# Performance work log

Hardware: AMD Instinct MI355X
Metric: run time of the kernel (lower is better)

Reference implementation:

```python
import jax, jax.numpy as jnp
import numpy as np

N = 50000
E = 800000
F = 128
H = 128
D = 3

def setup_inputs() -> dict:
    key = jax.random.key(0)
    ks = jax.random.split(key, 12)
    s = lambda fan_in: 1.0 / np.sqrt(fan_in)
    return {
        "node": jax.random.normal(ks[0], (N, F), jnp.float32),
        "coordinate": jax.random.normal(ks[1], (N, D), jnp.float32),
        "edge_index": jax.random.randint(ks[2], (2, E), 0, N, jnp.int32),
        "We1": jax.random.normal(ks[3], (2 * F + 1, H), jnp.float32) * s(2 * F + 1),
        "be1": jnp.zeros((H,), jnp.float32),
        "We2": jax.random.normal(ks[4], (H, H), jnp.float32) * s(H),
        "be2": jnp.zeros((H,), jnp.float32),
        "Wx": jax.random.normal(ks[5], (H, 1), jnp.float32) * s(H),
        "bx": jnp.zeros((1,), jnp.float32),
        "Wh1": jax.random.normal(ks[6], (F + H, H), jnp.float32) * s(F + H),
        "bh1": jnp.zeros((H,), jnp.float32),
        "Wh2": jax.random.normal(ks[7], (H, F), jnp.float32) * s(H),
        "bh2": jnp.zeros((F,), jnp.float32),
    }

def reference(node, coordinate, edge_index, We1, be1, We2, be2, Wx, bx, Wh1, bh1, Wh2, bh2):
    src = edge_index[0]
    dst = edge_index[1]
    n = node.shape[0]
    # gather endpoint features / coords
    h_j = node[src]            # [E, F]
    h_i = node[dst]            # [E, F]
    dist = coordinate[dst] - coordinate[src]          # [E, D] = x_i - x_j
    sqdist = jnp.sum(dist * dist, axis=1, keepdims=True)  # [E, 1]
    # phi_e: Linear -> ReLU -> Linear
    e_in = jnp.concatenate([h_i, h_j, sqdist], axis=-1)    # [E, 2F+1]
    m_ij = jax.nn.relu(e_in @ We1 + be1) @ We2 + be2       # [E, H]
    # phi_x: Linear to scalar edge weight
    w_ij = m_ij @ Wx + bx                                  # [E, 1]
    vec = dist * w_ij                                      # [E, D]
    C = 1.0 / (n - 1)
    delta_x = jax.ops.segment_sum(vec, dst, num_segments=n) * C
    x_new = coordinate + delta_x
    # aggregate messages per target node (sum)
    m_i = jax.ops.segment_sum(m_ij, dst, num_segments=n)   # [N, H]
    # phi_h: Linear -> ReLU -> Linear
    h_in = jnp.concatenate([node, m_i], axis=1)            # [N, F+H]
    h_new = jax.nn.relu(h_in @ Wh1 + bh1) @ Wh2 + bh2      # [N, F]
    return (h_new, x_new)
```

## Files before the change

kernel.cpp:

```cpp
#include <hip/hip_runtime.h>
#include <stdint.h>

#define NN 50000
#define NE 800000
#define NBINS 50001
#define H_OUT_OFF 6400000

typedef float  f32x4  __attribute__((ext_vector_type(4)));
typedef short  bf16x8 __attribute__((ext_vector_type(8)));

static __device__ __forceinline__ unsigned short f2b(float f) {
  unsigned u = __float_as_uint(f);
  return (unsigned short)((u + 0x7fffu + ((u >> 16) & 1u)) >> 16);
}
static __device__ __forceinline__ float b2f(unsigned short h) {
  return __uint_as_float(((unsigned)h) << 16);
}

__global__ void k1_kernel(const int* __restrict__ ei,
                          int* __restrict__ cnt,
                          unsigned short* __restrict__ rank,
                          const float* __restrict__ We1,
                          const float* __restrict__ We2,
                          const float* __restrict__ Wh1,
                          const float* __restrict__ Wh2,
                          const float* __restrict__ be2,
                          const float* __restrict__ Wx,
                          const float* __restrict__ bx,
                          unsigned short* __restrict__ We1Ttop,
                          unsigned short* __restrict__ We1Tbot,
                          unsigned short* __restrict__ We2T,
                          unsigned short* __restrict__ Wh1T,
                          unsigned short* __restrict__ Wh2T,
                          float* __restrict__ uvec) {
  int b = blockIdx.x, tid = threadIdx.x;
  if (b < 3125) {
    int i = b * 256 + tid;
    if (i < NE) rank[i] = (unsigned short)atomicAdd(&cnt[ei[NE + i]], 1);
    return;
  }
  b -= 3125;
  if (b < 384) {
    int i = b * 256 + tid;
    if (i < 16384) {
      int n = i >> 7, k = i & 127;
      We1Ttop[i] = f2b(We1[k * 128 + n]);
    } else if (i < 32768) {
      int j = i - 16384; int n = j >> 7, k = j & 127;
      We1Tbot[j] = f2b(We1[(128 + k) * 128 + n]);
    } else if (i < 49152) {
      int j = i - 32768; int n = j >> 7, k = j & 127;
      We2T[j] = f2b(We2[k * 128 + n]);
    } else if (i < 81920) {
      int j = i - 49152; int n = j >> 8, k = j & 255;
      Wh1T[j] = f2b(Wh1[k * 128 + n]);
    } else if (i < 98304) {
      int j = i - 81920; int n = j >> 7, k = j & 127;
      Wh2T[j] = f2b(Wh2[k * 128 + n]);
    }
    return;
  }
  int k = tid;
  if (k < 128) {
    float s = 0.f;
    for (int n = 0; n < 128; n++) s += We2[k * 128 + n] * Wx[n];
    uvec[k] = s;
  } else if (k == 128) {
    float s = 0.f;
    for (int n = 0; n < 128; n++) s += be2[n] * Wx[n];
    uvec[128] = s + bx[0];
  }
}

__global__ void scanA_kernel(const int* __restrict__ cnt, int* __restrict__ bsum) {
  __shared__ int sd[256];
  int b = blockIdx.x, t = threadIdx.x, i = b * 256 + t;
  sd[t] = (i < NBINS) ? cnt[i] : 0;
  __syncthreads();
  for (int s = 128; s; s >>= 1) {
    if (t < s) sd[t] += sd[t + s];
    __syncthreads();
  }
  if (t == 0) bsum[b] = sd[0];
}

__global__ void scanC_kernel(const int* __restrict__ cnt, const int* __restrict__ bsum,
                             int* __restrict__ starts) {
  __shared__ int sd[256];
  int b = blockIdx.x, t = threadIdx.x, i = b * 256 + t;
  int bv = (t < 196) ? bsum[t] : 0;
  sd[t] = bv;
  __syncthreads();
  for (int off = 1; off < 256; off <<= 1) {
    int x = (t >= off) ? sd[t - off] : 0;
    __syncthreads();
    sd[t] += x;
    __syncthreads();
  }
  int boff = (b > 0) ? sd[b - 1] : 0;
  __syncthreads();
  int v = (i < NBINS) ? cnt[i] : 0;
  sd[t] = v;
  __syncthreads();
  for (int off = 1; off < 256; off <<= 1) {
    int x = (t >= off) ? sd[t - off] : 0;
    __syncthreads();
    sd[t] += x;
    __syncthreads();
  }
  if (i < NBINS) starts[i] = sd[t] - v + boff;
}

__global__ __launch_bounds__(256, 4)
void k3_kernel(const int* __restrict__ ei,
               const unsigned short* __restrict__ rank,
               const int* __restrict__ starts,
               unsigned short* __restrict__ srcs,
               const float* __restrict__ node,
               const unsigned short* __restrict__ We1Ttop,
               const unsigned short* __restrict__ We1Tbot,
               const float* __restrict__ be1,
               unsigned short* __restrict__ Yb,
               unsigned short* __restrict__ Zb) {
  __shared__ __align__(16) unsigned short sA[64][136];
  const int tid = threadIdx.x;
  int b = blockIdx.x;

  if (b < 3125) {
    int i = b * 256 + tid;
    if (i < NE) {
      srcs[starts[ei[NE + i]] + (int)rank[i]] = (unsigned short)ei[i];
    }
    return;
  }
  b -= 3125;
  const int n0 = b * 64;

  for (int c = tid; c < 64 * 16; c += 256) {
    int e = c >> 4, s = c & 15;
    int n = n0 + e;
    if (n < NN) {
      const float* p = node + (size_t)n * 128 + s * 8;
      float4 v0 = *(const float4*)p;
      float4 v1 = *(const float4*)(p + 4);
      *(ushort4*)&sA[e][s * 8]     = make_ushort4(f2b(v0.x), f2b(v0.y), f2b(v0.z), f2b(v0.w));
      *(ushort4*)&sA[e][s * 8 + 4] = make_ushort4(f2b(v1.x), f2b(v1.y), f2b(v1.z), f2b(v1.w));
    } else {
      *(uint4*)&sA[e][s * 8] = make_uint4(0, 0, 0, 0);
    }
  }
  __syncthreads();

  const int wave = tid >> 6, lane = tid & 63;
  const int quad = lane >> 4, l16 = lane & 15;
  const int col0 = wave * 32 + l16, col1 = wave * 32 + 16 + l16;

  const f32x4 zero = {0.f, 0.f, 0.f, 0.f};
  f32x4 accY[4][2], accZ[4][2];
#pragma unroll
  for (int mt = 0; mt < 4; mt++) {
    accY[mt][0] = zero; accY[mt][1] = zero;
    accZ[mt][0] = zero; accZ[mt][1] = zero;
  }

#pragma unroll
  for (int kt = 0; kt < 4; kt++) {
    int kb = kt * 32 + quad * 8;
    bf16x8 by0 = *(const bf16x8*)(We1Ttop + (col0 << 7) + kb);
    bf16x8 by1 = *(const bf16x8*)(We1Ttop + (col1 << 7) + kb);
    bf16x8 bz0 = *(const bf16x8*)(We1Tbot + (col0 << 7) + kb);
    bf16x8 bz1 = *(const bf16x8*)(We1Tbot + (col1 << 7) + kb);
#pragma unroll
    for (int mt = 0; mt < 4; mt++) {
      bf16x8 a = *(const bf16x8*)&sA[mt * 16 + l16][kb];
      accY[mt][0] = __builtin_amdgcn_mfma_f32_16x16x32_bf16(a, by0, accY[mt][0], 0, 0, 0);
      accY[mt][1] = __builtin_amdgcn_mfma_f32_16x16x32_bf16(a, by1, accY[mt][1], 0, 0, 0);
      accZ[mt][0] = __builtin_amdgcn_mfma_f32_16x16x32_bf16(a, bz0, accZ[mt][0], 0, 0, 0);
      accZ[mt][1] = __builtin_amdgcn_mfma_f32_16x16x32_bf16(a, bz1, accZ[mt][1], 0, 0, 0);
    }
  }

  float sb0 = be1[col0], sb1 = be1[col1];
#pragma unroll
  for (int mt = 0; mt < 4; mt++) {
#pragma unroll
    for (int r = 0; r < 4; r++) {
      int row = mt * 16 + quad * 4 + r;
      int n = n0 + row;
      if (n < NN) {
        Yb[(size_t)n * 128 + col0] = f2b(accY[mt][0][r] + sb0);
        Yb[(size_t)n * 128 + col1] = f2b(accY[mt][1][r] + sb1);
        Zb[(size_t)n * 128 + col0] = f2b(accZ[mt][0][r]);
        Zb[(size_t)n * 128 + col1] = f2b(accZ[mt][1][r]);
      }
    }
  }
}

__global__ __launch_bounds__(256, 8)
void edge_kernel(const unsigned short* __restrict__ Zb,
                 const unsigned short* __restrict__ Yb,
                 const unsigned short* __restrict__ srcs,
                 const int* __restrict__ starts,
                 const float* __restrict__ coord,
                 const float* __restrict__ We1,
                 const float* __restrict__ uvec,
                 float* __restrict__ T,
                 float* __restrict__ out) {
  __shared__ int    sSrc[4][64];
  __shared__ float4 sQ[4][64];

  const int tid = threadIdx.x, wave = tid >> 6, lane = tid & 63;
  const int n = blockIdx.x * 4 + wave;
  const int half = lane >> 5, l32 = lane & 31;
  const int col = l32 * 4;

  const int start = starts[n], end = starts[n + 1];

  const float4 wsq = *(const float4*)(We1 + 256 * 128 + col);
  const float4 u   = *(const float4*)(uvec + col);
  const float  c   = uvec[128];
  ushort4 yv = *(const ushort4*)(Yb + (size_t)n * 128 + col);
  const float y0 = b2f(yv.x), y1 = b2f(yv.y), y2 = b2f(yv.z), y3 = b2f(yv.w);
  const float cdx = coord[n * 3 + 0], cdy = coord[n * 3 + 1], cdz = coord[n * 3 + 2];

  float aT0 = 0.f, aT1 = 0.f, aT2 = 0.f, aT3 = 0.f;
  float sx = 0.f, sy = 0.f, sz = 0.f;
  float dsx = 0.f, dsy = 0.f, dsz = 0.f;

  for (int cb = start; cb < end; cb += 64) {
    int m = end - cb; if (m > 64) m = 64;
    int s = 0; float dx = 0.f, dy = 0.f, dz = 0.f;
    if (lane < m) {
      s = (int)srcs[cb + lane];
      dx = cdx - coord[s * 3 + 0];
      dy = cdy - coord[s * 3 + 1];
      dz = cdz - coord[s * 3 + 2];
      dsx += dx; dsy += dy; dsz += dz;
    }
    sSrc[wave][lane] = s;
    sQ[wave][lane] = make_float4(dx, dy, dz, dx * dx + dy * dy + dz * dz);
    __builtin_amdgcn_wave_barrier();
    int pairs = (m + 1) >> 1;
    for (int p = 0; p < pairs; p++) {
      int idx = 2 * p + half;
      int ss = sSrc[wave][idx];
      float4 q = sQ[wave][idx];
      float valid = (idx < m) ? 1.f : 0.f;
      ushort4 zv = *(const ushort4*)(Zb + (size_t)ss * 128 + col);
      float t0 = fmaxf(b2f(zv.x) + y0 + q.w * wsq.x, 0.f) * valid;
      float t1 = fmaxf(b2f(zv.y) + y1 + q.w * wsq.y, 0.f) * valid;
      float t2 = fmaxf(b2f(zv.z) + y2 + q.w * wsq.z, 0.f) * valid;
      float t3 = fmaxf(b2f(zv.w) + y3 + q.w * wsq.w, 0.f) * valid;
      aT0 += t0; aT1 += t1; aT2 += t2; aT3 += t3;
      float tu = t0 * u.x + t1 * u.y + t2 * u.z + t3 * u.w;
      sx += tu * q.x; sy += tu * q.y; sz += tu * q.z;
    }
    __builtin_amdgcn_wave_barrier();
  }

  aT0 += __shfl_xor(aT0, 32); aT1 += __shfl_xor(aT1, 32);
  aT2 += __shfl_xor(aT2, 32); aT3 += __shfl_xor(aT3, 32);
  if (half == 0) {
    *(float4*)&T[(size_t)n * 128 + col] = make_float4(aT0, aT1, aT2, aT3);
  }

  float px = sx + c * dsx, py = sy + c * dsy, pz = sz + c * dsz;
#pragma unroll
  for (int o = 1; o < 64; o <<= 1) {
    px += __shfl_xor(px, o); py += __shfl_xor(py, o); pz += __shfl_xor(pz, o);
  }
  if (lane == 0) {
    const float C = 1.0f / 49999.0f;
    out[H_OUT_OFF + n * 3 + 0] = cdx + C * px;
    out[H_OUT_OFF + n * 3 + 1] = cdy + C * py;
    out[H_OUT_OFF + n * 3 + 2] = cdz + C * pz;
  }
}

__global__ __launch_bounds__(256, 3)
void node_kernel(const float* __restrict__ node,
                 const float* __restrict__ T,
                 const int* __restrict__ starts,
                 const unsigned short* __restrict__ We2T,
                 const float* __restrict__ be2,
                 const unsigned short* __restrict__ Wh1T,
                 const float* __restrict__ bh1,
                 const unsigned short* __restrict__ Wh2T,
                 const float* __restrict__ bh2,
                 float* __restrict__ out) {
  __shared__ __align__(16) unsigned short sA[64][264];
  __shared__ __align__(16) unsigned short sT[64][136];
  __shared__ float sDeg[64];

  const int tid = threadIdx.x;
  const int n0 = blockIdx.x * 64;

  if (tid < 64) {
    int n = n0 + tid;
    sDeg[tid] = (n < NN) ? (float)(starts[n + 1] - starts[n]) : 0.f;
  }

  for (int c = tid; c < 64 * 16; c += 256) {
    int e = c >> 4, s = c & 15;
    int n = n0 + e;
    if (n < NN) {
      const float* pn = node + (size_t)n * 128 + s * 8;
      float4 a0 = *(const float4*)pn;
      float4 a1 = *(const float4*)(pn + 4);
      *(ushort4*)&sA[e][s * 8]     = make_ushort4(f2b(a0.x), f2b(a0.y), f2b(a0.z), f2b(a0.w));
      *(ushort4*)&sA[e][s * 8 + 4] = make_ushort4(f2b(a1.x), f2b(a1.y), f2b(a1.z), f2b(a1.w));
      const float* p = T + (size_t)n * 128 + s * 8;
      float4 v0 = *(const float4*)p;
      float4 v1 = *(const float4*)(p + 4);
      *(ushort4*)&sT[e][s * 8]     = make_ushort4(f2b(v0.x), f2b(v0.y), f2b(v0.z), f2b(v0.w));
      *(ushort4*)&sT[e][s * 8 + 4] = make_ushort4(f2b(v1.x), f2b(v1.y), f2b(v1.z), f2b(v1.w));
    } else {
      *(uint4*)&sA[e][s * 8] = make_uint4(0, 0, 0, 0);
      *(uint4*)&sT[e][s * 8] = make_uint4(0, 0, 0, 0);
    }
  }
  __syncthreads();

  const int wave = tid >> 6, lane = tid & 63;
  const int quad = lane >> 4, l16 = lane & 15;
  const int col0 = wave * 32 + l16, col1 = wave * 32 + 16 + l16;

  const f32x4 zero = {0.f, 0.f, 0.f, 0.f};

  f32x4 accM[4][2];
#pragma unroll
  for (int mt = 0; mt < 4; mt++) { accM[mt][0] = zero; accM[mt][1] = zero; }
#pragma unroll
  for (int kt = 0; kt < 4; kt++) {
    int kb = kt * 32 + quad * 8;
    bf16x8 b0 = *(const bf16x8*)(We2T + (col0 << 7) + kb);
    bf16x8 b1 = *(const bf16x8*)(We2T + (col1 << 7) + kb);
#pragma unroll
    for (int mt = 0; mt < 4; mt++) {
      bf16x8 a = *(const bf16x8*)&sT[mt * 16 + l16][kb];
      accM[mt][0] = __builtin_amdgcn_mfma_f32_16x16x32_bf16(a, b0, accM[mt][0], 0, 0, 0);
      accM[mt][1] = __builtin_amdgcn_mfma_f32_16x16x32_bf16(a, b1, accM[mt][1], 0, 0, 0);
    }
  }
  {
    float eb0 = be2[col0], eb1 = be2[col1];
#pragma unroll
    for (int mt = 0; mt < 4; mt++) {
#pragma unroll
      for (int r = 0; r < 4; r++) {
        int row = mt * 16 + quad * 4 + r;
        float dg = sDeg[row];
        sA[row][128 + col0] = f2b(accM[mt][0][r] + dg * eb0);
        sA[row][128 + col1] = f2b(accM[mt][1][r] + dg * eb1);
      }
    }
  }
  __syncthreads();

  f32x4 acc[4][2];
#pragma unroll
  for (int mt = 0; mt < 4; mt++) { acc[mt][0] = zero; acc[mt][1] = zero; }
#pragma unroll
  for (int kt = 0; kt < 8; kt++) {
    int kb = kt * 32 + quad * 8;
    bf16x8 b0 = *(const bf16x8*)(Wh1T + (col0 << 8) + kb);
    bf16x8 b1 = *(const bf16x8*)(Wh1T + (col1 << 8) + kb);
#pragma unroll
    for (int mt = 0; mt < 4; mt++) {
      bf16x8 a = *(const bf16x8*)&sA[mt * 16 + l16][kb];
      acc[mt][0] = __builtin_amdgcn_mfma_f32_16x16x32_bf16(a, b0, acc[mt][0], 0, 0, 0);
      acc[mt][1] = __builtin_amdgcn_mfma_f32_16x16x32_bf16(a, b1, acc[mt][1], 0, 0, 0);
    }
  }
  {
    float sb0 = bh1[col0], sb1 = bh1[col1];
#pragma unroll
    for (int mt = 0; mt < 4; mt++) {
#pragma unroll
      for (int r = 0; r < 4; r++) {
        int row = mt * 16 + quad * 4 + r;
        sT[row][col0] = f2b(fmaxf(acc[mt][0][r] + sb0, 0.f));
        sT[row][col1] = f2b(fmaxf(acc[mt][1][r] + sb1, 0.f));
      }
    }
  }
  __syncthreads();

  f32x4 acc2[4][2];
#pragma unroll
  for (int mt = 0; mt < 4; mt++) { acc2[mt][0] = zero; acc2[mt][1] = zero; }
#pragma unroll
  for (int kt = 0; kt < 4; kt++) {
    int kb = kt * 32 + quad * 8;
    bf16x8 b0 = *(const bf16x8*)(Wh2T + (col0 << 7) + kb);
    bf16x8 b1 = *(const bf16x8*)(Wh2T + (col1 << 7) + kb);
#pragma unroll
    for (int mt = 0; mt < 4; mt++) {
      bf16x8 a = *(const bf16x8*)&sT[mt * 16 + l16][kb];
      acc2[mt][0] = __builtin_amdgcn_mfma_f32_16x16x32_bf16(a, b0, acc2[mt][0], 0, 0, 0);
      acc2[mt][1] = __builtin_amdgcn_mfma_f32_16x16x32_bf16(a, b1, acc2[mt][1], 0, 0, 0);
    }
  }
  {
    float eb0 = bh2[col0], eb1 = bh2[col1];
#pragma unroll
    for (int mt = 0; mt < 4; mt++) {
#pragma unroll
      for (int r = 0; r < 4; r++) {
        int row = mt * 16 + quad * 4 + r;
        int n = n0 + row;
        if (n < NN) {
          out[(size_t)n * 128 + col0] = acc2[mt][0][r] + eb0;
          out[(size_t)n * 128 + col1] = acc2[mt][1][r] + eb1;
        }
      }
    }
  }
}

extern "C" void kernel_launch(void* const* d_in, const int* in_sizes, int n_in,
                              void* d_out, int out_size, void* d_ws, size_t ws_size,
                              hipStream_t stream) {
  const float* node  = (const float*)d_in[0];
  const float* coord = (const float*)d_in[1];
  const int*   ei    = (const int*)d_in[2];
  const float* We1   = (const float*)d_in[3];
  const float* be1   = (const float*)d_in[4];
  const float* We2   = (const float*)d_in[5];
  const float* be2   = (const float*)d_in[6];
  const float* Wx    = (const float*)d_in[7];
  const float* bx    = (const float*)d_in[8];
  const float* Wh1   = (const float*)d_in[9];
  const float* bh1   = (const float*)d_in[10];
  const float* Wh2   = (const float*)d_in[11];
  const float* bh2   = (const float*)d_in[12];
  float* out = (float*)d_out;

  char* ws = (char*)d_ws;
  float*          T      = (float*)(ws);
  int*            cnt    = (int*)  (ws + 25600000);
  int*            starts = (int*)  (ws + 25800704);
  int*            bsum   = (int*)  (ws + 26001408);
  unsigned short* rank   = (unsigned short*)(ws + 26002432);
  unsigned short* srcs   = (unsigned short*)(ws + 27602432);
  unsigned short* Yb     = (unsigned short*)(ws + 29202432);
  unsigned short* Zb     = (unsigned short*)(ws + 42002432);
  unsigned short* We1Ttop= (unsigned short*)(ws + 54802432);
  unsigned short* We1Tbot= (unsigned short*)(ws + 54835200);
  unsigned short* We2T   = (unsigned short*)(ws + 54867968);
  unsigned short* Wh1T   = (unsigned short*)(ws + 54900736);
  unsigned short* Wh2T   = (unsigned short*)(ws + 54966272);
  float*          uvec   = (float*)(ws + 54999040);

  hipMemsetAsync(cnt, 0, 200704, stream);

  k1_kernel<<<3510, 256, 0, stream>>>(ei, cnt, rank, We1, We2, Wh1, Wh2,
                                      be2, Wx, bx,
                                      We1Ttop, We1Tbot, We2T, Wh1T, Wh2T, uvec);
  scanA_kernel<<<196, 256, 0, stream>>>(cnt, bsum);
  scanC_kernel<<<196, 256, 0, stream>>>(cnt, bsum, starts);
  k3_kernel<<<3907, 256, 0, stream>>>(ei, rank, starts, srcs,
                                      node, We1Ttop, We1Tbot, be1, Yb, Zb);
  edge_kernel<<<NN / 4, 256, 0, stream>>>(Zb, Yb, srcs, starts, coord, We1, uvec,
                                          T, out);
  node_kernel<<<782, 256, 0, stream>>>(node, T, starts, We2T, be2,
                                       Wh1T, bh1, Wh2T, bh2, out);
}
```

Baseline: 242.0 us.

## Fuse edge aggregation into node MLP kernel, keeping aggregates in shared memory

Merges the per-node edge aggregation kernel with the node MLP kernel. Each block first gathers and sums messages for its 64 nodes (one wave per 16 nodes sequentially), writing the aggregated bf16 features into shared memory alongside the node features. It then runs the MLP chain, which removes the fp32 T round-trip through global memory and one launch. The trade is far fewer waves working on the latency-bound gather, plus extra barriers from reusing the shared buffer.

```diff
diff --git a/kernel.cpp b/kernel.cpp
--- a/kernel.cpp
+++ b/kernel.cpp
@@ -17,15 +17,11 @@
   return __uint_as_float(((unsigned)h) << 16);
 }
 
-__global__ void k1_kernel(const int* __restrict__ ei,
-                          int* __restrict__ cnt,
+__global__ void k1_kernel(const int* __restrict__ ei, int* __restrict__ cnt,
                           unsigned short* __restrict__ rank,
-                          const float* __restrict__ We1,
-                          const float* __restrict__ We2,
-                          const float* __restrict__ Wh1,
-                          const float* __restrict__ Wh2,
-                          const float* __restrict__ be2,
-                          const float* __restrict__ Wx,
+                          const float* __restrict__ We1, const float* __restrict__ We2,
+                          const float* __restrict__ Wh1, const float* __restrict__ Wh2,
+                          const float* __restrict__ be2, const float* __restrict__ Wx,
                           const float* __restrict__ bx,
                           unsigned short* __restrict__ We1Ttop,
                           unsigned short* __restrict__ We1Tbot,
@@ -112,30 +108,23 @@
 }
 
 __global__ __launch_bounds__(256, 4)
-void k3_kernel(const int* __restrict__ ei,
-               const unsigned short* __restrict__ rank,
-               const int* __restrict__ starts,
-               unsigned short* __restrict__ srcs,
+void k3_kernel(const int* __restrict__ ei, const unsigned short* __restrict__ rank,
+               const int* __restrict__ starts, unsigned short* __restrict__ srcs,
                const float* __restrict__ node,
                const unsigned short* __restrict__ We1Ttop,
                const unsigned short* __restrict__ We1Tbot,
                const float* __restrict__ be1,
-               unsigned short* __restrict__ Yb,
-               unsigned short* __restrict__ Zb) {
+               unsigned short* __restrict__ Yb, unsigned short* __restrict__ Zb) {
   __shared__ __align__(16) unsigned short sA[64][136];
   const int tid = threadIdx.x;
   int b = blockIdx.x;
-
   if (b < 3125) {
     int i = b * 256 + tid;
-    if (i < NE) {
-      srcs[starts[ei[NE + i]] + (int)rank[i]] = (unsigned short)ei[i];
-    }
+    if (i < NE) srcs[starts[ei[NE + i]] + (int)rank[i]] = (unsigned short)ei[i];
     return;
   }
   b -= 3125;
   const int n0 = b * 64;
-
   for (int c = tid; c < 64 * 16; c += 256) {
     int e = c >> 4, s = c & 15;
     int n = n0 + e;
@@ -150,11 +139,9 @@
     }
   }
   __syncthreads();
-
   const int wave = tid >> 6, lane = tid & 63;
   const int quad = lane >> 4, l16 = lane & 15;
   const int col0 = wave * 32 + l16, col1 = wave * 32 + 16 + l16;
-
   const f32x4 zero = {0.f, 0.f, 0.f, 0.f};
   f32x4 accY[4][2], accZ[4][2];
 #pragma unroll
@@ -162,7 +149,6 @@
     accY[mt][0] = zero; accY[mt][1] = zero;
     accZ[mt][0] = zero; accZ[mt][1] = zero;
   }
-
 #pragma unroll
   for (int kt = 0; kt < 4; kt++) {
     int kb = kt * 32 + quad * 8;
@@ -179,7 +165,6 @@
       accZ[mt][1] = __builtin_amdgcn_mfma_f32_16x16x32_bf16(a, bz1, accZ[mt][1], 0, 0, 0);
     }
   }
-
   float sb0 = be1[col0], sb1 = be1[col1];
 #pragma unroll
   for (int mt = 0; mt < 4; mt++) {
@@ -197,109 +182,29 @@
   }
 }
 
-__global__ __launch_bounds__(256, 8)
-void edge_kernel(const unsigned short* __restrict__ Zb,
-                 const unsigned short* __restrict__ Yb,
-                 const unsigned short* __restrict__ srcs,
-                 const int* __restrict__ starts,
-                 const float* __restrict__ coord,
-                 const float* __restrict__ We1,
-                 const float* __restrict__ uvec,
-                 float* __restrict__ T,
-                 float* __restrict__ out) {
+__global__ __launch_bounds__(256, 4)
+void en_kernel(const unsigned short* __restrict__ Zb,
+               const unsigned short* __restrict__ Yb,
+               const unsigned short* __restrict__ srcs,
+               const int* __restrict__ starts,
+               const float* __restrict__ coord,
+               const float* __restrict__ We1,
+               const float* __restrict__ uvec,
+               const float* __restrict__ node,
+               const unsigned short* __restrict__ We2T,
+               const float* __restrict__ be2,
+               const unsigned short* __restrict__ Wh1T,
+               const float* __restrict__ bh1,
+               const unsigned short* __restrict__ Wh2T,
+               const float* __restrict__ bh2,
+               float* __restrict__ out) {
+  __shared__ __align__(16) unsigned short sA[64][264];
+  __shared__ float  sDeg[64];
   __shared__ int    sSrc[4][64];
   __shared__ float4 sQ[4][64];
 
   const int tid = threadIdx.x, wave = tid >> 6, lane = tid & 63;
-  const int n = blockIdx.x * 4 + wave;
-  const int half = lane >> 5, l32 = lane & 31;
-  const int col = l32 * 4;
-
-  const int start = starts[n], end = starts[n + 1];
-
-  const float4 wsq = *(const float4*)(We1 + 256 * 128 + col);
-  const float4 u   = *(const float4*)(uvec + col);
-  const float  c   = uvec[128];
-  ushort4 yv = *(const ushort4*)(Yb + (size_t)n * 128 + col);
-  const float y0 = b2f(yv.x), y1 = b2f(yv.y), y2 = b2f(yv.z), y3 = b2f(yv.w);
-  const float cdx = coord[n * 3 + 0], cdy = coord[n * 3 + 1], cdz = coord[n * 3 + 2];
-
-  float aT0 = 0.f, aT1 = 0.f, aT2 = 0.f, aT3 = 0.f;
-  float sx = 0.f, sy = 0.f, sz = 0.f;
-  float dsx = 0.f, dsy = 0.f, dsz = 0.f;
-
-  for (int cb = start; cb < end; cb += 64) {
-    int m = end - cb; if (m > 64) m = 64;
-    int s = 0; float dx = 0.f, dy = 0.f, dz = 0.f;
-    if (lane < m) {
-      s = (int)srcs[cb + lane];
-      dx = cdx - coord[s * 3 + 0];
-      dy = cdy - coord[s * 3 + 1];
-      dz = cdz - coord[s * 3 + 2];
-      dsx += dx; dsy += dy; dsz += dz;
-    }
-    sSrc[wave][lane] = s;
-    sQ[wave][lane] = make_float4(dx, dy, dz, dx * dx + dy * dy + dz * dz);
-    __builtin_amdgcn_wave_barrier();
-    int pairs = (m + 1) >> 1;
-    for (int p = 0; p < pairs; p++) {
-      int idx = 2 * p + half;
-      int ss = sSrc[wave][idx];
-      float4 q = sQ[wave][idx];
-      float valid = (idx < m) ? 1.f : 0.f;
-      ushort4 zv = *(const ushort4*)(Zb + (size_t)ss * 128 + col);
-      float t0 = fmaxf(b2f(zv.x) + y0 + q.w * wsq.x, 0.f) * valid;
-      float t1 = fmaxf(b2f(zv.y) + y1 + q.w * wsq.y, 0.f) * valid;
-      float t2 = fmaxf(b2f(zv.z) + y2 + q.w * wsq.z, 0.f) * valid;
-      float t3 = fmaxf(b2f(zv.w) + y3 + q.w * wsq.w, 0.f) * valid;
-      aT0 += t0; aT1 += t1; aT2 += t2; aT3 += t3;
-      float tu = t0 * u.x + t1 * u.y + t2 * u.z + t3 * u.w;
-      sx += tu * q.x; sy += tu * q.y; sz += tu * q.z;
-    }
-    __builtin_amdgcn_wave_barrier();
-  }
-
-  aT0 += __shfl_xor(aT0, 32); aT1 += __shfl_xor(aT1, 32);
-  aT2 += __shfl_xor(aT2, 32); aT3 += __shfl_xor(aT3, 32);
-  if (half == 0) {
-    *(float4*)&T[(size_t)n * 128 + col] = make_float4(aT0, aT1, aT2, aT3);
-  }
-
-  float px = sx + c * dsx, py = sy + c * dsy, pz = sz + c * dsz;
-#pragma unroll
-  for (int o = 1; o < 64; o <<= 1) {
-    px += __shfl_xor(px, o); py += __shfl_xor(py, o); pz += __shfl_xor(pz, o);
-  }
-  if (lane == 0) {
-    const float C = 1.0f / 49999.0f;
-    out[H_OUT_OFF + n * 3 + 0] = cdx + C * px;
-    out[H_OUT_OFF + n * 3 + 1] = cdy + C * py;
-    out[H_OUT_OFF + n * 3 + 2] = cdz + C * pz;
-  }
-}
-
-__global__ __launch_bounds__(256, 3)
-void node_kernel(const float* __restrict__ node,
-                 const float* __restrict__ T,
-                 const int* __restrict__ starts,
-                 const unsigned short* __restrict__ We2T,
-                 const float* __restrict__ be2,
-                 const unsigned short* __restrict__ Wh1T,
-                 const float* __restrict__ bh1,
-                 const unsigned short* __restrict__ Wh2T,
-                 const float* __restrict__ bh2,
-                 float* __restrict__ out) {
-  __shared__ __align__(16) unsigned short sA[64][264];
-  __shared__ __align__(16) unsigned short sT[64][136];
-  __shared__ float sDeg[64];
-
-  const int tid = threadIdx.x;
   const int n0 = blockIdx.x * 64;
-
-  if (tid < 64) {
-    int n = n0 + tid;
-    sDeg[tid] = (n < NN) ? (float)(starts[n + 1] - starts[n]) : 0.f;
-  }
 
   for (int c = tid; c < 64 * 16; c += 256) {
     int e = c >> 4, s = c & 15;
@@ -310,22 +215,93 @@
       float4 a1 = *(const float4*)(pn + 4);
       *(ushort4*)&sA[e][s * 8]     = make_ushort4(f2b(a0.x), f2b(a0.y), f2b(a0.z), f2b(a0.w));
       *(ushort4*)&sA[e][s * 8 + 4] = make_ushort4(f2b(a1.x), f2b(a1.y), f2b(a1.z), f2b(a1.w));
-      const float* p = T + (size_t)n * 128 + s * 8;
-      float4 v0 = *(const float4*)p;
-      float4 v1 = *(const float4*)(p + 4);
-      *(ushort4*)&sT[e][s * 8]     = make_ushort4(f2b(v0.x), f2b(v0.y), f2b(v0.z), f2b(v0.w));
-      *(ushort4*)&sT[e][s * 8 + 4] = make_ushort4(f2b(v1.x), f2b(v1.y), f2b(v1.z), f2b(v1.w));
     } else {
       *(uint4*)&sA[e][s * 8] = make_uint4(0, 0, 0, 0);
-      *(uint4*)&sT[e][s * 8] = make_uint4(0, 0, 0, 0);
-    }
-  }
-  __syncthreads();
-
-  const int wave = tid >> 6, lane = tid & 63;
+    }
+  }
+
+  {
+    const int half = lane >> 5, l32 = lane & 31;
+    const int col = l32 * 4;
+    const float4 wsq = *(const float4*)(We1 + 256 * 128 + col);
+    const float4 u   = *(const float4*)(uvec + col);
+    const float  cc  = uvec[128];
+
+    for (int r16 = 0; r16 < 16; r16++) {
+      const int row = (wave << 4) + r16;
+      const int n = n0 + row;
+      if (n < NN) {
+        const int start = starts[n], end = starts[n + 1];
+        ushort4 yv = *(const ushort4*)(Yb + (size_t)n * 128 + col);
+        const float y0 = b2f(yv.x), y1 = b2f(yv.y), y2 = b2f(yv.z), y3 = b2f(yv.w);
+        const float cdx = coord[n * 3 + 0], cdy = coord[n * 3 + 1], cdz = coord[n * 3 + 2];
+
+        float aT0 = 0.f, aT1 = 0.f, aT2 = 0.f, aT3 = 0.f;
+        float sx = 0.f, sy = 0.f, sz = 0.f;
+        float dsx = 0.f, dsy = 0.f, dsz = 0.f;
+
+        for (int cb = start; cb < end; cb += 64) {
+          int m = end - cb; if (m > 64) m = 64;
+          int s = 0; float dx = 0.f, dy = 0.f, dz = 0.f;
+          if (lane < m) {
+            s = (int)srcs[cb + lane];
+            dx = cdx - coord[s * 3 + 0];
+            dy = cdy - coord[s * 3 + 1];
+            dz = cdz - coord[s * 3 + 2];
+            dsx += dx; dsy += dy; dsz += dz;
+          }
+          sSrc[wave][lane] = s;
+          sQ[wave][lane] = make_float4(dx, dy, dz, dx * dx + dy * dy + dz * dz);
+          __builtin_amdgcn_wave_barrier();
+          int pairs = (m + 1) >> 1;
+          for (int p = 0; p < pairs; p++) {
+            int idx = 2 * p + half;
+            int ss = sSrc[wave][idx];
+            float4 q = sQ[wave][idx];
+            float valid = (idx < m) ? 1.f : 0.f;
+            ushort4 zv = *(const ushort4*)(Zb + (size_t)ss * 128 + col);
+            float t0 = fmaxf(b2f(zv.x) + y0 + q.w * wsq.x, 0.f) * valid;
+            float t1 = fmaxf(b2f(zv.y) + y1 + q.w * wsq.y, 0.f) * valid;
+            float t2 = fmaxf(b2f(zv.z) + y2 + q.w * wsq.z, 0.f) * valid;
+            float t3 = fmaxf(b2f(zv.w) + y3 + q.w * wsq.w, 0.f) * valid;
+            aT0 += t0; aT1 += t1; aT2 += t2; aT3 += t3;
+            float tu = t0 * u.x + t1 * u.y + t2 * u.z + t3 * u.w;
+            sx += tu * q.x; sy += tu * q.y; sz += tu * q.z;
+          }
+          __builtin_amdgcn_wave_barrier();
+        }
+
+        aT0 += __shfl_xor(aT0, 32); aT1 += __shfl_xor(aT1, 32);
+        aT2 += __shfl_xor(aT2, 32); aT3 += __shfl_xor(aT3, 32);
+        if (half == 0) {
+          *(ushort4*)&sA[row][128 + col] =
+              make_ushort4(f2b(aT0), f2b(aT1), f2b(aT2), f2b(aT3));
+        }
+        if (lane == 0) sDeg[row] = (float)(end - start);
+
+        float px = sx + cc * dsx, py = sy + cc * dsy, pz = sz + cc * dsz;
+#pragma unroll
+        for (int o = 1; o < 64; o <<= 1) {
+          px += __shfl_xor(px, o); py += __shfl_xor(py, o); pz += __shfl_xor(pz, o);
+        }
+        if (lane == 0) {
+          const float C = 1.0f / 49999.0f;
+          out[H_OUT_OFF + n * 3 + 0] = cdx + C * px;
+          out[H_OUT_OFF + n * 3 + 1] = cdy + C * py;
+          out[H_OUT_OFF + n * 3 + 2] = cdz + C * pz;
+        }
+      } else {
+        if ((lane >> 5) == 0) {
+          *(ushort4*)&sA[row][128 + (lane & 31) * 4] = make_ushort4(0, 0, 0, 0);
+        }
+        if (lane == 0) sDeg[row] = 0.f;
+      }
+    }
+  }
+  __syncthreads();
+
   const int quad = lane >> 4, l16 = lane & 15;
   const int col0 = wave * 32 + l16, col1 = wave * 32 + 16 + l16;
-
   const f32x4 zero = {0.f, 0.f, 0.f, 0.f};
 
   f32x4 accM[4][2];
@@ -338,11 +314,12 @@
     bf16x8 b1 = *(const bf16x8*)(We2T + (col1 << 7) + kb);
 #pragma unroll
     for (int mt = 0; mt < 4; mt++) {
-      bf16x8 a = *(const bf16x8*)&sT[mt * 16 + l16][kb];
+      bf16x8 a = *(const bf16x8*)&sA[mt * 16 + l16][128 + kb];
       accM[mt][0] = __builtin_amdgcn_mfma_f32_16x16x32_bf16(a, b0, accM[mt][0], 0, 0, 0);
       accM[mt][1] = __builtin_amdgcn_mfma_f32_16x16x32_bf16(a, b1, accM[mt][1], 0, 0, 0);
     }
   }
+  __syncthreads();
   {
     float eb0 = be2[col0], eb1 = be2[col1];
 #pragma unroll
@@ -373,6 +350,7 @@
       acc[mt][1] = __builtin_amdgcn_mfma_f32_16x16x32_bf16(a, b1, acc[mt][1], 0, 0, 0);
     }
   }
+  __syncthreads();
   {
     float sb0 = bh1[col0], sb1 = bh1[col1];
 #pragma unroll
@@ -380,8 +358,8 @@
 #pragma unroll
       for (int r = 0; r < 4; r++) {
         int row = mt * 16 + quad * 4 + r;
-        sT[row][col0] = f2b(fmaxf(acc[mt][0][r] + sb0, 0.f));
-        sT[row][col1] = f2b(fmaxf(acc[mt][1][r] + sb1, 0.f));
+        sA[row][col0] = f2b(fmaxf(acc[mt][0][r] + sb0, 0.f));
+        sA[row][col1] = f2b(fmaxf(acc[mt][1][r] + sb1, 0.f));
       }
     }
   }
@@ -397,7 +375,7 @@
     bf16x8 b1 = *(const bf16x8*)(Wh2T + (col1 << 7) + kb);
 #pragma unroll
     for (int mt = 0; mt < 4; mt++) {
-      bf16x8 a = *(const bf16x8*)&sT[mt * 16 + l16][kb];
+      bf16x8 a = *(const bf16x8*)&sA[mt * 16 + l16][kb];
       acc2[mt][0] = __builtin_amdgcn_mfma_f32_16x16x32_bf16(a, b0, acc2[mt][0], 0, 0, 0);
       acc2[mt][1] = __builtin_amdgcn_mfma_f32_16x16x32_bf16(a, b1, acc2[mt][1], 0, 0, 0);
     }
@@ -438,20 +416,19 @@
   float* out = (float*)d_out;
 
   char* ws = (char*)d_ws;
-  float*          T      = (float*)(ws);
-  int*            cnt    = (int*)  (ws + 25600000);
-  int*            starts = (int*)  (ws + 25800704);
-  int*            bsum   = (int*)  (ws + 26001408);
-  unsigned short* rank   = (unsigned short*)(ws + 26002432);
-  unsigned short* srcs   = (unsigned short*)(ws + 27602432);
-  unsigned short* Yb     = (unsigned short*)(ws + 29202432);
-  unsigned short* Zb     = (unsigned short*)(ws + 42002432);
-  unsigned short* We1Ttop= (unsigned short*)(ws + 54802432);
-  unsigned short* We1Tbot= (unsigned short*)(ws + 54835200);
-  unsigned short* We2T   = (unsigned short*)(ws + 54867968);
-  unsigned short* Wh1T   = (unsigned short*)(ws + 54900736);
-  unsigned short* Wh2T   = (unsigned short*)(ws + 54966272);
-  float*          uvec   = (float*)(ws + 54999040);
+  int*            cnt    = (int*)  (ws);
+  int*            starts = (int*)  (ws + 200704);
+  int*            bsum   = (int*)  (ws + 401408);
+  unsigned short* rank   = (unsigned short*)(ws + 402432);
+  unsigned short* srcs   = (unsigned short*)(ws + 2002432);
+  unsigned short* Yb     = (unsigned short*)(ws + 3602432);
+  unsigned short* Zb     = (unsigned short*)(ws + 16402432);
+  unsigned short* We1Ttop= (unsigned short*)(ws + 29202432);
+  unsigned short* We1Tbot= (unsigned short*)(ws + 29235200);
+  unsigned short* We2T   = (unsigned short*)(ws + 29267968);
+  unsigned short* Wh1T   = (unsigned short*)(ws + 29300736);
+  unsigned short* Wh2T   = (unsigned short*)(ws + 29366272);
+  float*          uvec   = (float*)(ws + 29399040);
 
   hipMemsetAsync(cnt, 0, 200704, stream);
 
@@ -462,8 +439,6 @@
   scanC_kernel<<<196, 256, 0, stream>>>(cnt, bsum, starts);
   k3_kernel<<<3907, 256, 0, stream>>>(ei, rank, starts, srcs,
                                       node, We1Ttop, We1Tbot, be1, Yb, Zb);
-  edge_kernel<<<NN / 4, 256, 0, stream>>>(Zb, Yb, srcs, starts, coord, We1, uvec,
-                                          T, out);
-  node_kernel<<<782, 256, 0, stream>>>(node, T, starts, We2T, be2,
-                                       Wh1T, bh1, Wh2T, bh2, out);
-}
+  en_kernel<<<782, 256, 0, stream>>>(Zb, Yb, srcs, starts, coord, We1, uvec,
+                                     node, We2T, be2, Wh1T, bh1, Wh2T, bh2, out);
+}
```

Measured after the change: 273.7 us. 1.13x slower.
